# Kernel optimization log

Hardware: AMD Instinct MI355X
Metric: run time of the kernel (lower is better)

Reference implementation:

```python
import jax, jax.numpy as jnp
import numpy as np

DIM = 1024
H = 16
DH = DIM // H
SCALE = DH ** -0.5
EPS = 1e-5


def _linear_params(key, fan_in, fan_out):
    k1, k2 = jax.random.split(key)
    bound = 1.0 / np.sqrt(fan_in)
    w = jax.random.uniform(k1, (fan_out, fan_in), jnp.float32, -bound, bound)
    b = jax.random.uniform(k2, (fan_out,), jnp.float32, -bound, bound)
    return w, b


def setup_inputs() -> dict:
    key = jax.random.key(0)
    ks = jax.random.split(key, 16)
    M, K, S_txt, S_img = 32, 128, 1024, 768
    inp = {
        'entity_text': jax.random.normal(ks[0], (M, K, DIM), jnp.float32),
        'entity_image': jax.random.normal(ks[1], (M, K, DIM), jnp.float32),
        'img_feat': jax.random.normal(ks[2], (M, S_img, DIM), jnp.float32),
        'txt_feat': jax.random.normal(ks[3], (M, S_txt, DIM), jnp.float32),
    }
    img_mask = jax.random.randint(ks[4], (M, S_img), 0, 2, jnp.int32)
    txt_mask = jax.random.randint(ks[5], (M, S_txt), 0, 2, jnp.int32)
    # guarantee at least one valid kv token per row (avoids all -inf rows)
    inp['img_mask'] = img_mask.at[:, 0].set(1)
    inp['txt_mask'] = txt_mask.at[:, 0].set(1)
    names = ['wq_t', 'wk_t', 'wv_t', 'wo_t', 'wq_i', 'wk_i', 'wv_i', 'wo_i']
    for i, n in enumerate(names):
        w, b = _linear_params(ks[6 + i], DIM, DIM)
        inp[n] = w
        inp['b' + n[1:]] = b
    inp['g_t'] = jnp.ones((DIM,), jnp.float32)
    inp['beta_t'] = jnp.zeros((DIM,), jnp.float32)
    inp['g_i'] = jnp.ones((DIM,), jnp.float32)
    inp['beta_i'] = jnp.zeros((DIM,), jnp.float32)
    return inp


def _attend(wq, bq, wk, bk, wv, bv, wo, bo, queries, kv, kv_mask):
    M, K, D = queries.shape
    S = kv.shape[1]
    Q = (queries @ wq.T + bq).reshape(M, K, H, DH)
    Kt = (kv @ wk.T + bk).reshape(M, S, H, DH)
    V = (kv @ wv.T + bv).reshape(M, S, H, DH)
    attn = jnp.einsum('mkhd,mshd->mhks', Q, Kt) * SCALE  # [M,H,K,S]
    attn = jnp.where(kv_mask[:, None, None, :] > 0, attn, -jnp.inf)
    attn = jax.nn.softmax(attn, axis=-1)
    attn = jnp.nan_to_num(attn, nan=0.0)  # dropout=eval mode (identity)
    out = jnp.einsum('mhks,mshd->mkhd', attn, V).reshape(M, K, D)
    return out @ wo.T + bo


def _layernorm(x, g, b):
    mu = jnp.mean(x, axis=-1, keepdims=True)
    var = jnp.mean(jnp.square(x - mu), axis=-1, keepdims=True)
    return (x - mu) * jax.lax.rsqrt(var + EPS) * g + b


def reference(entity_text, entity_image, img_feat, txt_feat, img_mask, txt_mask,
              wq_t, bq_t, wk_t, bk_t, wv_t, bv_t, wo_t, bo_t,
              wq_i, bq_i, wk_i, bk_i, wv_i, bv_i, wo_i, bo_i,
              g_t, beta_t, g_i, beta_i):
    out_t = _attend(wq_t, bq_t, wk_t, bk_t, wv_t, bv_t, wo_t, bo_t,
                    entity_text, txt_feat, txt_mask)
    out_i = _attend(wq_i, bq_i, wk_i, bk_i, wv_i, bv_i, wo_i, bo_i,
                    entity_image, img_feat, img_mask)
    et = _layernorm(entity_text + out_t, g_t, beta_t)
    ei = _layernorm(entity_image + out_i, g_i, beta_i)
    return (et, ei)
```

## Files before the change

### kernel.cpp

```cpp
#include <hip/hip_runtime.h>
#include <stdint.h>

typedef unsigned short u16;
typedef __attribute__((ext_vector_type(8))) short short8;
typedef __attribute__((ext_vector_type(4))) float f32x4;

#define SWZ(r) (((r) & 7) << 4)
#define SWZV(dr) ((((dr) & 7) ^ (((dr) >> 3) & 7)) << 4)
#define SCALE 0.125f

__device__ __forceinline__ u16 f2bf(float f) {
  unsigned int x = __float_as_uint(f);
  x += 0x7fffu + ((x >> 16) & 1u);
  return (u16)(x >> 16);
}

__device__ __forceinline__ unsigned int cvtpk_bf16(float lo, float hi) {
  unsigned int r;
  asm("v_cvt_pk_bf16_f32 %0, %1, %2" : "=v"(r) : "v"(lo), "v"(hi));
  return r;
}

__device__ __forceinline__ f32x4 mfma16(short8 a, short8 b, f32x4 c) {
  return __builtin_amdgcn_mfma_f32_16x16x32_bf16(a, b, c, 0, 0, 0);
}

__device__ __forceinline__ void gload_lds16(const u16* g, u16* l) {
  __builtin_amdgcn_global_load_lds(
      (const __attribute__((address_space(1))) unsigned int*)g,
      (__attribute__((address_space(3))) unsigned int*)l, 16, 0, 0);
}

__device__ __forceinline__ int xcd_swz(int bid, int nwg) {
  int cpx = nwg >> 3;
  return (bid & 7) * cpx + (bid >> 3);
}

__device__ __forceinline__ void cvt8(const float* src, u16* dst) {
  float4 a = *(const float4*)src;
  float4 b = *(const float4*)(src + 4);
  uint4 u;
  u.x = cvtpk_bf16(a.x, a.y);
  u.y = cvtpk_bf16(a.z, a.w);
  u.z = cvtpk_bf16(b.x, b.y);
  u.w = cvtpk_bf16(b.z, b.w);
  *(uint4*)dst = u;
}

__global__ __launch_bounds__(256) void cvt_all_kernel(
    const float* __restrict__ w0, const float* __restrict__ w1,
    const float* __restrict__ w2, const float* __restrict__ w3,
    const float* __restrict__ ent, const float* __restrict__ feat,
    u16* __restrict__ Wbf, u16* __restrict__ entbf, u16* __restrict__ featbf,
    int nE8, int nF8) {
  const int nW8 = 524288;
  int total = nW8 + nE8 + nF8;
  int i = blockIdx.x * 256 + threadIdx.x;
  int stride = gridDim.x * 256;
  for (; i < total; i += stride) {
    if (i < nW8) {
      int mi = i >> 17;
      const float* s = (mi == 0) ? w0 : (mi == 1) ? w1 : (mi == 2) ? w2 : w3;
      size_t off = (size_t)(i & 131071) * 8;
      cvt8(s + off, Wbf + (size_t)mi * 1048576 + off);
    } else if (i < nW8 + nE8) {
      size_t off = (size_t)(i - nW8) * 8;
      cvt8(ent + off, entbf + off);
    } else {
      size_t off = (size_t)(i - nW8 - nE8) * 8;
      cvt8(feat + off, featbf + off);
    }
  }
}

__global__ __launch_bounds__(256) void cvt_a_kernel(
    const float* __restrict__ src, u16* __restrict__ dst, int n8) {
  int i = blockIdx.x * 256 + threadIdx.x;
  int stride = gridDim.x * 256;
  for (; i < n8; i += stride) cvt8(src + (size_t)i * 8, dst + (size_t)i * 8);
}

__device__ __forceinline__ void gemm_core_bf16(
    const u16* __restrict__ A, const u16* __restrict__ B,
    const float* __restrict__ bias0, const float* __restrict__ bias1,
    u16* __restrict__ C, int ldc, int bx, int by, u16* As, u16* Bs) {
  const int tid = threadIdx.x;
  const int lane = tid & 63;
  const int w = tid >> 6;
  const int wr = w >> 1, wc = w & 1;
  const int l15 = lane & 15, lg = lane >> 4;
  const int brow = by * 128;
  const int bcol = bx * 128;

  f32x4 acc[4][4] = {};

  for (int k0 = 0; k0 < 1024; k0 += 64) {
#pragma unroll
    for (int p = 0; p < 4; ++p) {
      int flat = p * 256 + tid;
      int row = flat >> 3;
      int cb = (flat & 7) * 16;
      int scb = cb ^ SWZ(row);
      gload_lds16(B + (size_t)(bcol + row) * 1024 + k0 + (scb >> 1),
                  Bs + (size_t)flat * 8);
    }
#pragma unroll
    for (int p = 0; p < 4; ++p) {
      int flat = p * 256 + tid;
      int row = flat >> 3;
      int cb = (flat & 7) * 16;
      int scb = cb ^ SWZ(row);
      gload_lds16(A + (size_t)(brow + row) * 1024 + k0 + (scb >> 1),
                  As + (size_t)flat * 8);
    }
    __syncthreads();

    short8 af[4][2], bfr[4][2];
#pragma unroll
    for (int i = 0; i < 4; ++i) {
#pragma unroll
      for (int kk = 0; kk < 2; ++kk) {
        int ar = wr * 64 + i * 16 + l15;
        af[i][kk] = *(const short8*)((const char*)As + ar * 128 +
                                     ((kk * 64 + lg * 16) ^ SWZ(ar)));
        int br = wc * 64 + i * 16 + l15;
        bfr[i][kk] = *(const short8*)((const char*)Bs + br * 128 +
                                      ((kk * 64 + lg * 16) ^ SWZ(br)));
      }
    }
#pragma unroll
    for (int i = 0; i < 4; ++i)
#pragma unroll
      for (int j = 0; j < 4; ++j)
#pragma unroll
        for (int kk = 0; kk < 2; ++kk)
          acc[i][j] = mfma16(af[i][kk], bfr[j][kk], acc[i][j]);
    __syncthreads();
  }

#pragma unroll
  for (int j = 0; j < 4; ++j) {
    int col = bcol + wc * 64 + j * 16 + l15;
    const float* bp = (col < 1024) ? bias0 : bias1;
    float bv = bp[col & 1023];
#pragma unroll
    for (int i = 0; i < 4; ++i) {
      int row0 = brow + wr * 64 + i * 16 + lg * 4;
#pragma unroll
      for (int r = 0; r < 4; ++r)
        C[(size_t)(row0 + r) * ldc + col] = f2bf(acc[i][j][r] + bv);
    }
  }
}

__global__ __launch_bounds__(256, 2) void qkv_gemm_kernel(
    const u16* __restrict__ A0, const u16* __restrict__ B0,
    const float* __restrict__ bq, u16* __restrict__ C0, int gx0, int nwg0,
    const u16* __restrict__ A1, const u16* __restrict__ B1,
    const float* __restrict__ bk, const float* __restrict__ bv,
    u16* __restrict__ C1, int gx1, int nwg1) {
  __shared__ __attribute__((aligned(16))) u16 As[128 * 64];
  __shared__ __attribute__((aligned(16))) u16 Bs[128 * 64];
  int bid = blockIdx.x;
  if (bid < nwg0) {
    int lid = xcd_swz(bid, nwg0);
    gemm_core_bf16(A0, B0, bq, bq, C0, 1024, lid % gx0, lid / gx0, As, Bs);
  } else {
    int lid = xcd_swz(bid - nwg0, nwg1);
    gemm_core_bf16(A1, B1, bk, bv, C1, 2048, lid % gx1, lid / gx1, As, Bs);
  }
}

template <bool A_F32, bool OUT_F32>
__global__ __launch_bounds__(256, 2) void gemm_bias_kernel(
    const void* __restrict__ Av, const u16* __restrict__ B,
    const float* __restrict__ bias0, const float* __restrict__ bias1,
    void* __restrict__ Cv, int ldc) {
  __shared__ __attribute__((aligned(16))) u16 As[128 * 64];
  __shared__ __attribute__((aligned(16))) u16 Bs[128 * 64];
  const int tid = threadIdx.x;
  const int lane = tid & 63;
  const int w = tid >> 6;
  const int wr = w >> 1, wc = w & 1;
  const int l15 = lane & 15, lg = lane >> 4;

  const int nwg = gridDim.x * gridDim.y;
  const int lid = xcd_swz(blockIdx.y * gridDim.x + blockIdx.x, nwg);
  const int bx = lid % gridDim.x;
  const int by = lid / gridDim.x;
  const int brow = by * 128;
  const int bcol = bx * 128;

  f32x4 acc[4][4] = {};

  for (int k0 = 0; k0 < 1024; k0 += 64) {
#pragma unroll
    for (int p = 0; p < 4; ++p) {
      int flat = p * 256 + tid;
      int row = flat >> 3;
      int cb = (flat & 7) * 16;
      int scb = cb ^ SWZ(row);
      gload_lds16(B + (size_t)(bcol + row) * 1024 + k0 + (scb >> 1),
                  Bs + (size_t)flat * 8);
    }
    if constexpr (A_F32) {
      const float* Af = (const float*)Av;
#pragma unroll
      for (int p = 0; p < 4; ++p) {
        int flat = p * 256 + tid;
        int row = flat >> 3;
        int c8 = flat & 7;
        const float* src = Af + (size_t)(brow + row) * 1024 + k0 + c8 * 8;
        float4 v0 = ((const float4*)src)[0];
        float4 v1 = ((const float4*)src)[1];
        uint4 u;
        u.x = cvtpk_bf16(v0.x, v0.y);
        u.y = cvtpk_bf16(v0.z, v0.w);
        u.z = cvtpk_bf16(v1.x, v1.y);
        u.w = cvtpk_bf16(v1.z, v1.w);
        *(uint4*)((char*)As + row * 128 + ((c8 * 16) ^ SWZ(row))) = u;
      }
    } else {
      const u16* Ab = (const u16*)Av;
#pragma unroll
      for (int p = 0; p < 4; ++p) {
        int flat = p * 256 + tid;
        int row = flat >> 3;
        int cb = (flat & 7) * 16;
        int scb = cb ^ SWZ(row);
        gload_lds16(Ab + (size_t)(brow + row) * 1024 + k0 + (scb >> 1),
                    As + (size_t)flat * 8);
      }
    }
    __syncthreads();

    short8 af[4][2], bfr[4][2];
#pragma unroll
    for (int i = 0; i < 4; ++i) {
#pragma unroll
      for (int kk = 0; kk < 2; ++kk) {
        int ar = wr * 64 + i * 16 + l15;
        af[i][kk] = *(const short8*)((const char*)As + ar * 128 +
                                     ((kk * 64 + lg * 16) ^ SWZ(ar)));
        int br = wc * 64 + i * 16 + l15;
        bfr[i][kk] = *(const short8*)((const char*)Bs + br * 128 +
                                      ((kk * 64 + lg * 16) ^ SWZ(br)));
      }
    }
#pragma unroll
    for (int i = 0; i < 4; ++i)
#pragma unroll
      for (int j = 0; j < 4; ++j)
#pragma unroll
        for (int kk = 0; kk < 2; ++kk)
          acc[i][j] = mfma16(af[i][kk], bfr[j][kk], acc[i][j]);
    __syncthreads();
  }

#pragma unroll
  for (int j = 0; j < 4; ++j) {
    int col = bcol + wc * 64 + j * 16 + l15;
    const float* bp = (col < 1024) ? bias0 : bias1;
    float bv = bp[col & 1023];
#pragma unroll
    for (int i = 0; i < 4; ++i) {
      int row0 = brow + wr * 64 + i * 16 + lg * 4;
#pragma unroll
      for (int r = 0; r < 4; ++r) {
        float v = acc[i][j][r] + bv;
        if constexpr (OUT_F32)
          ((float*)Cv)[(size_t)(row0 + r) * ldc + col] = v;
        else
          ((u16*)Cv)[(size_t)(row0 + r) * ldc + col] = f2bf(v);
      }
    }
  }
}

__global__ __launch_bounds__(256, 2) void attn_mfma_kernel(
    const u16* __restrict__ Q, const u16* __restrict__ KV,
    const int* __restrict__ mask, u16* __restrict__ AO, int S, int mbase) {
  __shared__ __attribute__((aligned(16))) u16 Ks[64 * 64];
  __shared__ __attribute__((aligned(16))) u16 Vt[64 * 64];
  __shared__ __attribute__((aligned(16))) u16 Ps[4 * 32 * 64];
  __shared__ float mb[64];

  const int tid = threadIdx.x;
  const int lane = tid & 63;
  const int w = tid >> 6;
  const int lid = xcd_swz(blockIdx.x, gridDim.x);
  const int ml = lid >> 4;
  const int h = lid & 15;
  const int mg = mbase + ml;
  const int l15 = lane & 15, lg = lane >> 4;

  short8 qf[2][2];
#pragma unroll
  for (int qb = 0; qb < 2; ++qb)
#pragma unroll
    for (int kk = 0; kk < 2; ++kk)
      qf[qb][kk] = *(const short8*)(Q + (size_t)(mg * 128 + w * 32 + qb * 16 + l15) * 1024 +
                                    h * 64 + kk * 32 + lg * 8);

  float mrun[2][4], lrun[2][4];
  f32x4 oacc[2][4] = {};
#pragma unroll
  for (int qb = 0; qb < 2; ++qb)
#pragma unroll
    for (int r = 0; r < 4; ++r) {
      mrun[qb][r] = -1e30f;
      lrun[qb][r] = 0.0f;
    }

  const size_t kvbase = (size_t)ml * S * 2048 + h * 64;

  for (int st = 0; st < S; st += 64) {
    if (tid < 64)
      mb[tid] = (mask[(size_t)mg * S + st + tid] > 0) ? 0.0f : -1e30f;
#pragma unroll
    for (int p = 0; p < 2; ++p) {
      int flat = p * 256 + tid;
      int row = flat >> 3;
      int c = flat & 7;
      short8 v = *(const short8*)(KV + kvbase + (size_t)(st + row) * 2048 + c * 8);
      *(short8*)((char*)Ks + row * 128 + ((c * 16) ^ SWZ(row))) = v;
    }
    {
      int sp = (tid >> 3) * 2;
      int c = tid & 7;
      const u16* src = KV + kvbase + 1024 + (size_t)(st + sp) * 2048 + c * 8;
      short8 v0 = *(const short8*)(src);
      short8 v1 = *(const short8*)(src + 2048);
#pragma unroll
      for (int j = 0; j < 8; ++j) {
        int dr = c * 8 + j;
        unsigned int val = (unsigned int)(u16)v0[j] | ((unsigned int)(u16)v1[j] << 16);
        *(unsigned int*)((char*)Vt + dr * 128 + ((sp * 2) ^ SWZV(dr))) = val;
      }
    }
    __syncthreads();

    short8 kf[4][2];
#pragma unroll
    for (int sb = 0; sb < 4; ++sb)
#pragma unroll
      for (int kk = 0; kk < 2; ++kk) {
        int row = sb * 16 + l15;
        kf[sb][kk] = *(const short8*)((const char*)Ks + row * 128 +
                                      ((kk * 64 + lg * 16) ^ SWZ(row)));
      }
    f32x4 sc[2][4] = {};
#pragma unroll
    for (int qb = 0; qb < 2; ++qb)
#pragma unroll
      for (int sb = 0; sb < 4; ++sb)
#pragma unroll
        for (int kk = 0; kk < 2; ++kk)
          sc[qb][sb] = mfma16(qf[qb][kk], kf[sb][kk], sc[qb][sb]);

    float mbv[4];
#pragma unroll
    for (int sb = 0; sb < 4; ++sb) mbv[sb] = mb[sb * 16 + l15];

#pragma unroll
    for (int qb = 0; qb < 2; ++qb) {
#pragma unroll
      for (int r = 0; r < 4; ++r) {
        float s0 = sc[qb][0][r] * SCALE + mbv[0];
        float s1 = sc[qb][1][r] * SCALE + mbv[1];
        float s2 = sc[qb][2][r] * SCALE + mbv[2];
        float s3 = sc[qb][3][r] * SCALE + mbv[3];
        float t = fmaxf(fmaxf(s0, s1), fmaxf(s2, s3));
        for (int d = 1; d < 16; d <<= 1) t = fmaxf(t, __shfl_xor(t, d));
        float mnew = fmaxf(mrun[qb][r], t);
        float resc = __expf(mrun[qb][r] - mnew);
        float p0 = __expf(s0 - mnew);
        float p1 = __expf(s1 - mnew);
        float p2 = __expf(s2 - mnew);
        float p3 = __expf(s3 - mnew);
        float rs = p0 + p1 + p2 + p3;
        for (int d = 1; d < 16; d <<= 1) rs += __shfl_xor(rs, d);
        lrun[qb][r] = lrun[qb][r] * resc + rs;
        mrun[qb][r] = mnew;
#pragma unroll
        for (int db = 0; db < 4; ++db) oacc[qb][db][r] *= resc;
        int row = qb * 16 + lg * 4 + r;
        char* pbase = (char*)Ps + (w * 32 + row) * 128;
        int colb = 2 * l15;
        *(u16*)(pbase + ((0 * 32 + colb) ^ SWZ(row))) = f2bf(p0);
        *(u16*)(pbase + ((1 * 32 + colb) ^ SWZ(row))) = f2bf(p1);
        *(u16*)(pbase + ((2 * 32 + colb) ^ SWZ(row))) = f2bf(p2);
        *(u16*)(pbase + ((3 * 32 + colb) ^ SWZ(row))) = f2bf(p3);
      }
    }
    asm volatile("" ::: "memory");

    short8 pf[2][2], vf[4][2];
#pragma unroll
    for (int qb = 0; qb < 2; ++qb)
#pragma unroll
      for (int kk = 0; kk < 2; ++kk) {
        int row = qb * 16 + l15;
        pf[qb][kk] = *(const short8*)((const char*)Ps + (w * 32 + row) * 128 +
                                      ((kk * 64 + lg * 16) ^ SWZ(row)));
      }
#pragma unroll
    for (int db = 0; db < 4; ++db)
#pragma unroll
      for (int kk = 0; kk < 2; ++kk) {
        int row = db * 16 + l15;
        vf[db][kk] = *(const short8*)((const char*)Vt + row * 128 +
                                      ((kk * 64 + lg * 16) ^ SWZV(row)));
      }
#pragma unroll
    for (int qb = 0; qb < 2; ++qb)
#pragma unroll
      for (int db = 0; db < 4; ++db)
#pragma unroll
        for (int kk = 0; kk < 2; ++kk)
          oacc[qb][db] = mfma16(pf[qb][kk], vf[db][kk], oacc[qb][db]);
    __syncthreads();
  }

#pragma unroll
  for (int qb = 0; qb < 2; ++qb)
#pragma unroll
    for (int db = 0; db < 4; ++db)
#pragma unroll
      for (int r = 0; r < 4; ++r) {
        int grow = mg * 128 + w * 32 + qb * 16 + lg * 4 + r;
        int gcol = h * 64 + db * 16 + l15;
        float v = oacc[qb][db][r] / lrun[qb][r];
        AO[(size_t)grow * 1024 + gcol] = f2bf(v);
      }
}

__global__ __launch_bounds__(256) void ln_kernel(
    const float* __restrict__ X, const float* __restrict__ O,
    const float* __restrict__ g, const float* __restrict__ b,
    float* __restrict__ out) {
  int row = blockIdx.x;
  int tid = threadIdx.x;
  const float* xr = X + (size_t)row * 1024;
  const float* orr = O + (size_t)row * 1024;
  float4 xv = *(const float4*)(xr + tid * 4);
  float4 ov = *(const float4*)(orr + tid * 4);
  float v0 = xv.x + ov.x, v1 = xv.y + ov.y, v2 = xv.z + ov.z, v3 = xv.w + ov.w;
  float s = v0 + v1 + v2 + v3;
  float s2 = v0 * v0 + v1 * v1 + v2 * v2 + v3 * v3;
  for (int d = 1; d < 64; d <<= 1) {
    s += __shfl_xor(s, d);
    s2 += __shfl_xor(s2, d);
  }
  __shared__ float ps[4], ps2[4];
  int w = tid >> 6;
  if ((tid & 63) == 0) {
    ps[w] = s;
    ps2[w] = s2;
  }
  __syncthreads();
  s = ps[0] + ps[1] + ps[2] + ps[3];
  s2 = ps2[0] + ps2[1] + ps2[2] + ps2[3];
  float mu = s * (1.0f / 1024.0f);
  float var = s2 * (1.0f / 1024.0f) - mu * mu;
  float rstd = rsqrtf(var + 1e-5f);
  float4 gv = *(const float4*)(g + tid * 4);
  float4 bv = *(const float4*)(b + tid * 4);
  float4 ou;
  ou.x = (v0 - mu) * rstd * gv.x + bv.x;
  ou.y = (v1 - mu) * rstd * gv.y + bv.y;
  ou.z = (v2 - mu) * rstd * gv.z + bv.z;
  ou.w = (v3 - mu) * rstd * gv.w + bv.w;
  *(float4*)(out + (size_t)row * 1024 + tid * 4) = ou;
}

extern "C" void kernel_launch(void* const* d_in, const int* in_sizes, int n_in,
                              void* d_out, int out_size, void* d_ws, size_t ws_size,
                              hipStream_t stream) {
  const float* ent_t = (const float*)d_in[0];
  const float* ent_i = (const float*)d_in[1];
  const float* img_feat = (const float*)d_in[2];
  const float* txt_feat = (const float*)d_in[3];
  const int* img_mask = (const int*)d_in[4];
  const int* txt_mask = (const int*)d_in[5];
  const float* W[8];
  const float* Bv[8];
  for (int i = 0; i < 8; ++i) {
    W[i] = (const float*)d_in[6 + 2 * i];
    Bv[i] = (const float*)d_in[7 + 2 * i];
  }
  const float* g_t = (const float*)d_in[22];
  const float* beta_t = (const float*)d_in[23];
  const float* g_i = (const float*)d_in[24];
  const float* beta_i = (const float*)d_in[25];
  float* out = (float*)d_out;

  int nc = 0;
  size_t Xt = 0;
  for (int t = 1; t <= 4; t <<= 1) {
    size_t x = 134217728ull / t;
    if ((32ull << 20) + x + x / 2 <= ws_size) { nc = t; Xt = x; break; }
  }

  char* ws = (char*)d_ws;
  u16* Wbf = (u16*)ws;
  u16* Qbf = (u16*)(ws + (8ull << 20));
  u16* AObf = (u16*)(ws + (16ull << 20));

  if (nc > 0) {
    u16* entbf = (u16*)(ws + (24ull << 20));
    u16* KVc = (u16*)(ws + (32ull << 20));
    u16* featbf = (u16*)(ws + (32ull << 20) + Xt);
    float* Of32 = (float*)(ws + (32ull << 20));
    const int mpc = 32 / nc;

    for (int mod = 0; mod < 2; ++mod) {
      const float* ent = mod ? ent_i : ent_t;
      const float* feat = mod ? img_feat : txt_feat;
      const int* msk = mod ? img_mask : txt_mask;
      int S = mod ? 768 : 1024;
      int crows = mpc * S;

      const u16* wq = Wbf + 0ull * 1048576;
      const u16* wkv = Wbf + 1ull * 1048576;
      const u16* wo = Wbf + 3ull * 1048576;
      const float* bq = Bv[mod * 4 + 0];
      const float* bk = Bv[mod * 4 + 1];
      const float* bvv = Bv[mod * 4 + 2];
      const float* bo = Bv[mod * 4 + 3];

      cvt_all_kernel<<<2048, 256, 0, stream>>>(
          W[mod * 4 + 0], W[mod * 4 + 1], W[mod * 4 + 2], W[mod * 4 + 3],
          ent, feat, Wbf, entbf, featbf, 4096 * 128, crows * 128);

      for (int c = 0; c < nc; ++c) {
        if (c > 0) {
          const float* featc = feat + (size_t)c * mpc * S * 1024;
          cvt_a_kernel<<<2048, 256, 0, stream>>>(featc, featbf, crows * 128);
        }
        int nwg0 = (c == 0) ? 256 : 0;
        int nwg1 = 16 * (crows / 128);
        qkv_gemm_kernel<<<nwg0 + nwg1, 256, 0, stream>>>(
            entbf, wq, bq, Qbf, 8, nwg0,
            featbf, wkv, bk, bvv, KVc, 16, nwg1);
        attn_mfma_kernel<<<mpc * 16, 256, 0, stream>>>(Qbf, KVc, msk, AObf, S, c * mpc);
      }

      gemm_bias_kernel<false, true><<<dim3(8, 32), 256, 0, stream>>>(
          AObf, wo, bo, bo, Of32, 1024);
      ln_kernel<<<4096, 256, 0, stream>>>(ent, Of32,
                                          mod ? g_i : g_t, mod ? beta_i : beta_t,
                                          out + (size_t)mod * 4194304);
    }
  } else {
    int ncf = 4;
    if (ws_size >= (152ull << 20)) ncf = 1;
    else if (ws_size >= (88ull << 20)) ncf = 2;
    u16* KVc = (u16*)(ws + (24ull << 20));
    float* Of32 = (float*)(ws + (24ull << 20));
    const int mpc = 32 / ncf;

    for (int mod = 0; mod < 2; ++mod) {
      const float* ent = mod ? ent_i : ent_t;
      const float* feat = mod ? img_feat : txt_feat;
      const int* msk = mod ? img_mask : txt_mask;
      int S = mod ? 768 : 1024;

      cvt_all_kernel<<<2048, 256, 0, stream>>>(
          W[mod * 4 + 0], W[mod * 4 + 1], W[mod * 4 + 2], W[mod * 4 + 3],
          ent, ent, Wbf, Qbf, Qbf, 0, 0);

      const u16* wq = Wbf + 0ull * 1048576;
      const u16* wkv = Wbf + 1ull * 1048576;
      const u16* wo = Wbf + 3ull * 1048576;
      const float* bq = Bv[mod * 4 + 0];
      const float* bk = Bv[mod * 4 + 1];
      const float* bvv = Bv[mod * 4 + 2];
      const float* bo = Bv[mod * 4 + 3];

      gemm_bias_kernel<true, false><<<dim3(8, 32), 256, 0, stream>>>(
          ent, wq, bq, bq, Qbf, 1024);

      int crows = mpc * S;
      for (int c = 0; c < ncf; ++c) {
        const float* featc = feat + (size_t)c * mpc * S * 1024;
        gemm_bias_kernel<true, false><<<dim3(16, crows / 128), 256, 0, stream>>>(
            featc, wkv, bk, bvv, KVc, 2048);
        attn_mfma_kernel<<<mpc * 16, 256, 0, stream>>>(Qbf, KVc, msk, AObf, S, c * mpc);
      }

      gemm_bias_kernel<false, true><<<dim3(8, 32), 256, 0, stream>>>(
          AObf, wo, bo, bo, Of32, 1024);
      ln_kernel<<<4096, 256, 0, stream>>>(ent, Of32,
                                          mod ? g_i : g_t, mod ? beta_i : beta_t,
                                          out + (size_t)mod * 4194304);
    }
  }
}
```

Before: 511.7 us.

## Batch both modalities into shared QKV, attention, output-projection and layernorm launches

When the workspace holds at least 400MB, a new path converts both modalities up front and runs their Q/KV GEMMs, attention, output projection and layernorm as single combined launches rather than per-modality, chunked sequences. This cuts launch count and the tail idle time of small grids, and lets the two modalities' work fill the GPU together. In exchange it needs a much larger workspace, and the old chunked path is kept as a fallback when memory is short.

```diff
diff --git a/kernel.cpp b/kernel.cpp
--- a/kernel.cpp
+++ b/kernel.cpp
@@ -80,10 +80,11 @@
   for (; i < n8; i += stride) cvt8(src + (size_t)i * 8, dst + (size_t)i * 8);
 }
 
-__device__ __forceinline__ void gemm_core_bf16(
+template <bool OUT_F32>
+__device__ __forceinline__ void gemm_core(
     const u16* __restrict__ A, const u16* __restrict__ B,
     const float* __restrict__ bias0, const float* __restrict__ bias1,
-    u16* __restrict__ C, int ldc, int bx, int by, u16* As, u16* Bs) {
+    void* __restrict__ Cv, int ldc, int bx, int by, u16* As, u16* Bs) {
   const int tid = threadIdx.x;
   const int lane = tid & 63;
   const int w = tid >> 6;
@@ -99,8 +100,7 @@
     for (int p = 0; p < 4; ++p) {
       int flat = p * 256 + tid;
       int row = flat >> 3;
-      int cb = (flat & 7) * 16;
-      int scb = cb ^ SWZ(row);
+      int scb = ((flat & 7) * 16) ^ SWZ(row);
       gload_lds16(B + (size_t)(bcol + row) * 1024 + k0 + (scb >> 1),
                   Bs + (size_t)flat * 8);
     }
@@ -108,8 +108,7 @@
     for (int p = 0; p < 4; ++p) {
       int flat = p * 256 + tid;
       int row = flat >> 3;
-      int cb = (flat & 7) * 16;
-      int scb = cb ^ SWZ(row);
+      int scb = ((flat & 7) * 16) ^ SWZ(row);
       gload_lds16(A + (size_t)(brow + row) * 1024 + k0 + (scb >> 1),
                   As + (size_t)flat * 8);
     }
@@ -147,9 +146,43 @@
     for (int i = 0; i < 4; ++i) {
       int row0 = brow + wr * 64 + i * 16 + lg * 4;
 #pragma unroll
-      for (int r = 0; r < 4; ++r)
-        C[(size_t)(row0 + r) * ldc + col] = f2bf(acc[i][j][r] + bv);
-    }
+      for (int r = 0; r < 4; ++r) {
+        float v = acc[i][j][r] + bv;
+        if constexpr (OUT_F32)
+          ((float*)Cv)[(size_t)(row0 + r) * ldc + col] = v;
+        else
+          ((u16*)Cv)[(size_t)(row0 + r) * ldc + col] = f2bf(v);
+      }
+    }
+  }
+}
+
+__global__ __launch_bounds__(256, 2) void qkv4_kernel(
+    const u16* __restrict__ A0, const u16* __restrict__ B0,
+    const float* __restrict__ b0q, u16* __restrict__ C0, int n0,
+    const u16* __restrict__ A1, const u16* __restrict__ B1,
+    const float* __restrict__ b1k, const float* __restrict__ b1v,
+    u16* __restrict__ C1, int n1,
+    const u16* __restrict__ A2, const u16* __restrict__ B2,
+    const float* __restrict__ b2q, u16* __restrict__ C2, int n2,
+    const u16* __restrict__ A3, const u16* __restrict__ B3,
+    const float* __restrict__ b3k, const float* __restrict__ b3v,
+    u16* __restrict__ C3, int n3) {
+  __shared__ __attribute__((aligned(16))) u16 As[128 * 64];
+  __shared__ __attribute__((aligned(16))) u16 Bs[128 * 64];
+  int bid = blockIdx.x;
+  if (bid < n0) {
+    int lid = xcd_swz(bid, n0);
+    gemm_core<false>(A0, B0, b0q, b0q, C0, 1024, lid % 8, lid / 8, As, Bs);
+  } else if (bid < n0 + n1) {
+    int lid = xcd_swz(bid - n0, n1);
+    gemm_core<false>(A1, B1, b1k, b1v, C1, 2048, lid % 16, lid / 16, As, Bs);
+  } else if (bid < n0 + n1 + n2) {
+    int lid = xcd_swz(bid - n0 - n1, n2);
+    gemm_core<false>(A2, B2, b2q, b2q, C2, 1024, lid % 8, lid / 8, As, Bs);
+  } else {
+    int lid = xcd_swz(bid - n0 - n1 - n2, n3);
+    gemm_core<false>(A3, B3, b3k, b3v, C3, 2048, lid % 16, lid / 16, As, Bs);
   }
 }
 
@@ -164,10 +197,27 @@
   int bid = blockIdx.x;
   if (bid < nwg0) {
     int lid = xcd_swz(bid, nwg0);
-    gemm_core_bf16(A0, B0, bq, bq, C0, 1024, lid % gx0, lid / gx0, As, Bs);
+    gemm_core<false>(A0, B0, bq, bq, C0, 1024, lid % gx0, lid / gx0, As, Bs);
   } else {
     int lid = xcd_swz(bid - nwg0, nwg1);
-    gemm_core_bf16(A1, B1, bk, bv, C1, 2048, lid % gx1, lid / gx1, As, Bs);
+    gemm_core<false>(A1, B1, bk, bv, C1, 2048, lid % gx1, lid / gx1, As, Bs);
+  }
+}
+
+__global__ __launch_bounds__(256, 2) void wo2_kernel(
+    const u16* __restrict__ A0, const u16* __restrict__ B0,
+    const float* __restrict__ b0, float* __restrict__ C0, int n0,
+    const u16* __restrict__ A1, const u16* __restrict__ B1,
+    const float* __restrict__ b1, float* __restrict__ C1) {
+  __shared__ __attribute__((aligned(16))) u16 As[128 * 64];
+  __shared__ __attribute__((aligned(16))) u16 Bs[128 * 64];
+  int bid = blockIdx.x;
+  if (bid < n0) {
+    int lid = xcd_swz(bid, n0);
+    gemm_core<true>(A0, B0, b0, b0, C0, 1024, lid % 8, lid / 8, As, Bs);
+  } else {
+    int lid = xcd_swz(bid - n0, gridDim.x - n0);
+    gemm_core<true>(A1, B1, b1, b1, C1, 1024, lid % 8, lid / 8, As, Bs);
   }
 }
 
@@ -179,31 +229,31 @@
   __shared__ __attribute__((aligned(16))) u16 As[128 * 64];
   __shared__ __attribute__((aligned(16))) u16 Bs[128 * 64];
   const int tid = threadIdx.x;
-  const int lane = tid & 63;
-  const int w = tid >> 6;
-  const int wr = w >> 1, wc = w & 1;
-  const int l15 = lane & 15, lg = lane >> 4;
-
   const int nwg = gridDim.x * gridDim.y;
   const int lid = xcd_swz(blockIdx.y * gridDim.x + blockIdx.x, nwg);
   const int bx = lid % gridDim.x;
   const int by = lid / gridDim.x;
-  const int brow = by * 128;
-  const int bcol = bx * 128;
-
-  f32x4 acc[4][4] = {};
-
-  for (int k0 = 0; k0 < 1024; k0 += 64) {
-#pragma unroll
-    for (int p = 0; p < 4; ++p) {
-      int flat = p * 256 + tid;
-      int row = flat >> 3;
-      int cb = (flat & 7) * 16;
-      int scb = cb ^ SWZ(row);
-      gload_lds16(B + (size_t)(bcol + row) * 1024 + k0 + (scb >> 1),
-                  Bs + (size_t)flat * 8);
-    }
-    if constexpr (A_F32) {
+
+  if constexpr (!A_F32) {
+    gemm_core<OUT_F32>((const u16*)Av, B, bias0, bias1, Cv, ldc, bx, by, As, Bs);
+    return;
+  } else {
+    const int lane = tid & 63;
+    const int w = tid >> 6;
+    const int wr = w >> 1, wc = w & 1;
+    const int l15 = lane & 15, lg = lane >> 4;
+    const int brow = by * 128;
+    const int bcol = bx * 128;
+    f32x4 acc[4][4] = {};
+    for (int k0 = 0; k0 < 1024; k0 += 64) {
+#pragma unroll
+      for (int p = 0; p < 4; ++p) {
+        int flat = p * 256 + tid;
+        int row = flat >> 3;
+        int scb = ((flat & 7) * 16) ^ SWZ(row);
+        gload_lds16(B + (size_t)(bcol + row) * 1024 + k0 + (scb >> 1),
+                    Bs + (size_t)flat * 8);
+      }
       const float* Af = (const float*)Av;
 #pragma unroll
       for (int p = 0; p < 4; ++p) {
@@ -220,66 +270,54 @@
         u.w = cvtpk_bf16(v1.z, v1.w);
         *(uint4*)((char*)As + row * 128 + ((c8 * 16) ^ SWZ(row))) = u;
       }
-    } else {
-      const u16* Ab = (const u16*)Av;
-#pragma unroll
-      for (int p = 0; p < 4; ++p) {
-        int flat = p * 256 + tid;
-        int row = flat >> 3;
-        int cb = (flat & 7) * 16;
-        int scb = cb ^ SWZ(row);
-        gload_lds16(Ab + (size_t)(brow + row) * 1024 + k0 + (scb >> 1),
-                    As + (size_t)flat * 8);
-      }
-    }
-    __syncthreads();
-
-    short8 af[4][2], bfr[4][2];
-#pragma unroll
-    for (int i = 0; i < 4; ++i) {
-#pragma unroll
-      for (int kk = 0; kk < 2; ++kk) {
-        int ar = wr * 64 + i * 16 + l15;
-        af[i][kk] = *(const short8*)((const char*)As + ar * 128 +
-                                     ((kk * 64 + lg * 16) ^ SWZ(ar)));
-        int br = wc * 64 + i * 16 + l15;
-        bfr[i][kk] = *(const short8*)((const char*)Bs + br * 128 +
-                                      ((kk * 64 + lg * 16) ^ SWZ(br)));
-      }
-    }
-#pragma unroll
-    for (int i = 0; i < 4; ++i)
-#pragma unroll
-      for (int j = 0; j < 4; ++j)
-#pragma unroll
-        for (int kk = 0; kk < 2; ++kk)
-          acc[i][j] = mfma16(af[i][kk], bfr[j][kk], acc[i][j]);
-    __syncthreads();
-  }
-
-#pragma unroll
-  for (int j = 0; j < 4; ++j) {
-    int col = bcol + wc * 64 + j * 16 + l15;
-    const float* bp = (col < 1024) ? bias0 : bias1;
-    float bv = bp[col & 1023];
-#pragma unroll
-    for (int i = 0; i < 4; ++i) {
-      int row0 = brow + wr * 64 + i * 16 + lg * 4;
-#pragma unroll
-      for (int r = 0; r < 4; ++r) {
-        float v = acc[i][j][r] + bv;
-        if constexpr (OUT_F32)
-          ((float*)Cv)[(size_t)(row0 + r) * ldc + col] = v;
-        else
-          ((u16*)Cv)[(size_t)(row0 + r) * ldc + col] = f2bf(v);
-      }
-    }
-  }
-}
-
-__global__ __launch_bounds__(256, 2) void attn_mfma_kernel(
+      __syncthreads();
+      short8 af[4][2], bfr[4][2];
+#pragma unroll
+      for (int i = 0; i < 4; ++i) {
+#pragma unroll
+        for (int kk = 0; kk < 2; ++kk) {
+          int ar = wr * 64 + i * 16 + l15;
+          af[i][kk] = *(const short8*)((const char*)As + ar * 128 +
+                                       ((kk * 64 + lg * 16) ^ SWZ(ar)));
+          int br = wc * 64 + i * 16 + l15;
+          bfr[i][kk] = *(const short8*)((const char*)Bs + br * 128 +
+                                        ((kk * 64 + lg * 16) ^ SWZ(br)));
+        }
+      }
+#pragma unroll
+      for (int i = 0; i < 4; ++i)
+#pragma unroll
+        for (int j = 0; j < 4; ++j)
+#pragma unroll
+          for (int kk = 0; kk < 2; ++kk)
+            acc[i][j] = mfma16(af[i][kk], bfr[j][kk], acc[i][j]);
+      __syncthreads();
+    }
+#pragma unroll
+    for (int j = 0; j < 4; ++j) {
+      int col = bcol + wc * 64 + j * 16 + l15;
+      const float* bp = (col < 1024) ? bias0 : bias1;
+      float bv = bp[col & 1023];
+#pragma unroll
+      for (int i = 0; i < 4; ++i) {
+        int row0 = brow + wr * 64 + i * 16 + lg * 4;
+#pragma unroll
+        for (int r = 0; r < 4; ++r) {
+          float v = acc[i][j][r] + bv;
+          if constexpr (OUT_F32)
+            ((float*)Cv)[(size_t)(row0 + r) * ldc + col] = v;
+          else
+            ((u16*)Cv)[(size_t)(row0 + r) * ldc + col] = f2bf(v);
+        }
+      }
+    }
+  }
+}
+
+__device__ __forceinline__ void attn_core(
     const u16* __restrict__ Q, const u16* __restrict__ KV,
-    const int* __restrict__ mask, u16* __restrict__ AO, int S, int mbase) {
+    const int* __restrict__ mask, u16* __restrict__ AO, int S, int mbase,
+    int lid) {
   __shared__ __attribute__((aligned(16))) u16 Ks[64 * 64];
   __shared__ __attribute__((aligned(16))) u16 Vt[64 * 64];
   __shared__ __attribute__((aligned(16))) u16 Ps[4 * 32 * 64];
@@ -288,7 +326,6 @@
   const int tid = threadIdx.x;
   const int lane = tid & 63;
   const int w = tid >> 6;
-  const int lid = xcd_swz(blockIdx.x, gridDim.x);
   const int ml = lid >> 4;
   const int h = lid & 15;
   const int mg = mbase + ml;
@@ -435,11 +472,30 @@
       }
 }
 
-__global__ __launch_bounds__(256) void ln_kernel(
+__global__ __launch_bounds__(256, 2) void attn_mfma_kernel(
+    const u16* __restrict__ Q, const u16* __restrict__ KV,
+    const int* __restrict__ mask, u16* __restrict__ AO, int S, int mbase) {
+  int lid = xcd_swz(blockIdx.x, gridDim.x);
+  attn_core(Q, KV, mask, AO, S, mbase, lid);
+}
+
+__global__ __launch_bounds__(256, 2) void attn2_kernel(
+    const u16* __restrict__ Q0, const u16* __restrict__ KV0,
+    const int* __restrict__ m0, u16* __restrict__ AO0, int S0,
+    const u16* __restrict__ Q1, const u16* __restrict__ KV1,
+    const int* __restrict__ m1, u16* __restrict__ AO1, int S1) {
+  int bid = blockIdx.x;
+  if (bid < 512) {
+    attn_core(Q0, KV0, m0, AO0, S0, 0, xcd_swz(bid, 512));
+  } else {
+    attn_core(Q1, KV1, m1, AO1, S1, 0, xcd_swz(bid - 512, 512));
+  }
+}
+
+__device__ __forceinline__ void ln_core(
     const float* __restrict__ X, const float* __restrict__ O,
     const float* __restrict__ g, const float* __restrict__ b,
-    float* __restrict__ out) {
-  int row = blockIdx.x;
+    float* __restrict__ out, int row) {
   int tid = threadIdx.x;
   const float* xr = X + (size_t)row * 1024;
   const float* orr = O + (size_t)row * 1024;
@@ -474,6 +530,26 @@
   *(float4*)(out + (size_t)row * 1024 + tid * 4) = ou;
 }
 
+__global__ __launch_bounds__(256) void ln_kernel(
+    const float* __restrict__ X, const float* __restrict__ O,
+    const float* __restrict__ g, const float* __restrict__ b,
+    float* __restrict__ out) {
+  ln_core(X, O, g, b, out, blockIdx.x);
+}
+
+__global__ __launch_bounds__(256) void ln2_kernel(
+    const float* __restrict__ X0, const float* __restrict__ O0,
+    const float* __restrict__ g0, const float* __restrict__ b0,
+    const float* __restrict__ X1, const float* __restrict__ O1,
+    const float* __restrict__ g1, const float* __restrict__ b1,
+    float* __restrict__ out) {
+  int row = blockIdx.x;
+  if (row < 4096)
+    ln_core(X0, O0, g0, b0, out, row);
+  else
+    ln_core(X1, O1, g1, b1, out + 4194304, row - 4096);
+}
+
 extern "C" void kernel_launch(void* const* d_in, const int* in_sizes, int n_in,
                               void* d_out, int out_size, void* d_ws, size_t ws_size,
                               hipStream_t stream) {
@@ -494,6 +570,56 @@
   const float* g_i = (const float*)d_in[24];
   const float* beta_i = (const float*)d_in[25];
   float* out = (float*)d_out;
+  char* ws = (char*)d_ws;
+
+  if (ws_size >= (400ull << 20)) {
+    u16* Wbf = (u16*)ws;
+    u16* Qbf_t = (u16*)(ws + (16ull << 20));
+    u16* Qbf_i = (u16*)(ws + (24ull << 20));
+    u16* AObf_t = (u16*)(ws + (32ull << 20));
+    u16* AObf_i = (u16*)(ws + (40ull << 20));
+    u16* entbf_t = (u16*)(ws + (48ull << 20));
+    u16* entbf_i = (u16*)(ws + (56ull << 20));
+    u16* featbf_t = (u16*)(ws + (64ull << 20));
+    u16* featbf_i = (u16*)(ws + (128ull << 20));
+    u16* KVt = (u16*)(ws + (176ull << 20));
+    u16* KVi = (u16*)(ws + (304ull << 20));
+    float* Of32_t = (float*)(ws + (176ull << 20));
+    float* Of32_i = (float*)(ws + (192ull << 20));
+
+    const u16* wq_t = Wbf;
+    const u16* wkv_t = Wbf + 1ull * 1048576;
+    const u16* wo_t = Wbf + 3ull * 1048576;
+    const u16* wq_i = Wbf + 4ull * 1048576;
+    const u16* wkv_i = Wbf + 5ull * 1048576;
+    const u16* wo_i = Wbf + 7ull * 1048576;
+
+    cvt_all_kernel<<<2048, 256, 0, stream>>>(
+        W[0], W[1], W[2], W[3], ent_t, txt_feat,
+        Wbf, entbf_t, featbf_t, 524288, 4194304);
+    cvt_all_kernel<<<2048, 256, 0, stream>>>(
+        W[4], W[5], W[6], W[7], ent_i, img_feat,
+        Wbf + 4ull * 1048576, entbf_i, featbf_i, 524288, 3145728);
+
+    qkv4_kernel<<<256 + 4096 + 256 + 3072, 256, 0, stream>>>(
+        entbf_t, wq_t, Bv[0], Qbf_t, 256,
+        featbf_t, wkv_t, Bv[1], Bv[2], KVt, 4096,
+        entbf_i, wq_i, Bv[4], Qbf_i, 256,
+        featbf_i, wkv_i, Bv[5], Bv[6], KVi, 3072);
+
+    attn2_kernel<<<1024, 256, 0, stream>>>(
+        Qbf_t, KVt, txt_mask, AObf_t, 1024,
+        Qbf_i, KVi, img_mask, AObf_i, 768);
+
+    wo2_kernel<<<512, 256, 0, stream>>>(
+        AObf_t, wo_t, Bv[3], Of32_t, 256,
+        AObf_i, wo_i, Bv[7], Of32_i);
+
+    ln2_kernel<<<8192, 256, 0, stream>>>(
+        ent_t, Of32_t, g_t, beta_t,
+        ent_i, Of32_i, g_i, beta_i, out);
+    return;
+  }
 
   int nc = 0;
   size_t Xt = 0;
@@ -502,7 +628,6 @@
     if ((32ull << 20) + x + x / 2 <= ws_size) { nc = t; Xt = x; break; }
   }
 
-  char* ws = (char*)d_ws;
   u16* Wbf = (u16*)ws;
   u16* Qbf = (u16*)(ws + (8ull << 20));
   u16* AObf = (u16*)(ws + (16ull << 20));
@@ -521,13 +646,9 @@
       int S = mod ? 768 : 1024;
       int crows = mpc * S;
 
-      const u16* wq = Wbf + 0ull * 1048576;
+      const u16* wq = Wbf;
       const u16* wkv = Wbf + 1ull * 1048576;
       const u16* wo = Wbf + 3ull * 1048576;
-      const float* bq = Bv[mod * 4 + 0];
-      const float* bk = Bv[mod * 4 + 1];
-      const float* bvv = Bv[mod * 4 + 2];
-      const float* bo = Bv[mod * 4 + 3];
 
       cvt_all_kernel<<<2048, 256, 0, stream>>>(
           W[mod * 4 + 0], W[mod * 4 + 1], W[mod * 4 + 2], W[mod * 4 + 3],
@@ -541,13 +662,13 @@
         int nwg0 = (c == 0) ? 256 : 0;
         int nwg1 = 16 * (crows / 128);
         qkv_gemm_kernel<<<nwg0 + nwg1, 256, 0, stream>>>(
-            entbf, wq, bq, Qbf, 8, nwg0,
-            featbf, wkv, bk, bvv, KVc, 16, nwg1);
+            entbf, wq, Bv[mod * 4 + 0], Qbf, 8, nwg0,
+            featbf, wkv, Bv[mod * 4 + 1], Bv[mod * 4 + 2], KVc, 16, nwg1);
         attn_mfma_kernel<<<mpc * 16, 256, 0, stream>>>(Qbf, KVc, msk, AObf, S, c * mpc);
       }
 
       gemm_bias_kernel<false, true><<<dim3(8, 32), 256, 0, stream>>>(
-          AObf, wo, bo, bo, Of32, 1024);
+          AObf, wo, Bv[mod * 4 + 3], Bv[mod * 4 + 3], Of32, 1024);
       ln_kernel<<<4096, 256, 0, stream>>>(ent, Of32,
                                           mod ? g_i : g_t, mod ? beta_i : beta_t,
                                           out + (size_t)mod * 4194304);
@@ -570,27 +691,23 @@
           W[mod * 4 + 0], W[mod * 4 + 1], W[mod * 4 + 2], W[mod * 4 + 3],
           ent, ent, Wbf, Qbf, Qbf, 0, 0);
 
-      const u16* wq = Wbf + 0ull * 1048576;
+      const u16* wq = Wbf;
       const u16* wkv = Wbf + 1ull * 1048576;
       const u16* wo = Wbf + 3ull * 1048576;
-      const float* bq = Bv[mod * 4 + 0];
-      const float* bk = Bv[mod * 4 + 1];
-      const float* bvv = Bv[mod * 4 + 2];
-      const float* bo = Bv[mod * 4 + 3];
 
       gemm_bias_kernel<true, false><<<dim3(8, 32), 256, 0, stream>>>(
-          ent, wq, bq, bq, Qbf, 1024);
+          ent, wq, Bv[mod * 4 + 0], Bv[mod * 4 + 0], Qbf, 1024);
 
       int crows = mpc * S;
       for (int c = 0; c < ncf; ++c) {
         const float* featc = feat + (size_t)c * mpc * S * 1024;
         gemm_bias_kernel<true, false><<<dim3(16, crows / 128), 256, 0, stream>>>(
-            featc, wkv, bk, bvv, KVc, 2048);
+            featc, wkv, Bv[mod * 4 + 1], Bv[mod * 4 + 2], KVc, 2048);
         attn_mfma_kernel<<<mpc * 16, 256, 0, stream>>>(Qbf, KVc, msk, AObf, S, c * mpc);
       }
 
       gemm_bias_kernel<false, true><<<dim3(8, 32), 256, 0, stream>>>(
-          AObf, wo, bo, bo, Of32, 1024);
+          AObf, wo, Bv[mod * 4 + 3], Bv[mod * 4 + 3], Of32, 1024);
       ln_kernel<<<4096, 256, 0, stream>>>(ent, Of32,
                                           mod ? g_i : g_t, mod ? beta_i : beta_t,
                                           out + (size_t)mod * 4194304);
```

New measurement: 523.7 us. 1.02x slower.
